# Kernel tuning notes

Hardware: AMD Instinct MI355X
Metric: run time of the kernel (lower is better)

The kernel has to match this reference:

```python
import jax, jax.numpy as jnp
import numpy as np

N_EMBD = 1024
N_HEAD = 16
HEAD_DIM = N_EMBD // N_HEAD
B, T = 2, 2048


def setup_inputs() -> dict:
    key = jax.random.key(0)
    ks = jax.random.split(key, 12)
    s = 0.02
    inp = {
        "x": jax.random.normal(ks[0], (B, T, N_EMBD), dtype=jnp.float32),
        "ln1_g": jnp.ones((N_EMBD,), jnp.float32),
        "ln1_b": jnp.zeros((N_EMBD,), jnp.float32),
        "ln2_g": jnp.ones((N_EMBD,), jnp.float32),
        "ln2_b": jnp.zeros((N_EMBD,), jnp.float32),
        "W_qkv": jax.random.normal(ks[1], (N_EMBD, 3 * N_EMBD), jnp.float32) * s,
        "b_qkv": jnp.zeros((3 * N_EMBD,), jnp.float32),
        "W_o": jax.random.normal(ks[2], (N_EMBD, N_EMBD), jnp.float32) * s,
        "b_o": jnp.zeros((N_EMBD,), jnp.float32),
        "W_fc": jax.random.normal(ks[3], (N_EMBD, 4 * N_EMBD), jnp.float32) * s,
        "b_fc": jnp.zeros((4 * N_EMBD,), jnp.float32),
        "W_proj": jax.random.normal(ks[4], (4 * N_EMBD, N_EMBD), jnp.float32) * s,
        "b_proj": jnp.zeros((N_EMBD,), jnp.float32),
    }
    return inp


def _layernorm(x, g, b, eps=1e-5):
    mu = jnp.mean(x, axis=-1, keepdims=True)
    var = jnp.var(x, axis=-1, keepdims=True)
    return (x - mu) * jax.lax.rsqrt(var + eps) * g + b


def _block(x, ln1_g, ln1_b, ln2_g, ln2_b, W_qkv, b_qkv, W_o, b_o, W_fc, b_fc, W_proj, b_proj):
    # --- attention sub-block (pre-LN) ---
    h = _layernorm(x, ln1_g, ln1_b)
    qkv = h @ W_qkv + b_qkv                     # [B,T,3E]
    q, k, v = jnp.split(qkv, 3, axis=-1)
    def split_heads(t):
        return t.reshape(B, T, N_HEAD, HEAD_DIM).transpose(0, 2, 1, 3)  # [B,H,T,D]
    q, k, v = split_heads(q), split_heads(k), split_heads(v)
    scores = jnp.einsum("bhqd,bhkd->bhqk", q, k) / (HEAD_DIM ** 0.5)
    causal = jnp.tril(jnp.ones((T, T), dtype=bool))
    scores = jnp.where(causal, scores, jnp.float32(-jnp.inf))
    probs = jax.nn.softmax(scores, axis=-1)
    attn = jnp.einsum("bhqk,bhkd->bhqd", probs, v)        # [B,H,T,D]
    attn = attn.transpose(0, 2, 1, 3).reshape(B, T, N_EMBD)
    x = x + attn @ W_o + b_o
    # --- MLP sub-block (pre-LN) ---
    h = _layernorm(x, ln2_g, ln2_b)
    h = jax.nn.gelu(h @ W_fc + b_fc, approximate=False)
    x = x + h @ W_proj + b_proj
    return x


def reference(x, ln1_g, ln1_b, ln2_g, ln2_b, W_qkv, b_qkv, W_o, b_o, W_fc, b_fc, W_proj, b_proj):
    return _block(x, ln1_g, ln1_b, ln2_g, ln2_b, W_qkv, b_qkv, W_o, b_o, W_fc, b_fc, W_proj, b_proj)
```

## Files before the change

kernel.cpp:

```cpp
#include <hip/hip_runtime.h>
#include <hip/hip_bf16.h>


#define TT 2048
#define EE 1024
#define NH 16
#define HD 64

#define AS1 __attribute__((address_space(1)))
#define AS3 __attribute__((address_space(3)))

using bf16x8 = __bf16 __attribute__((ext_vector_type(8)));
using bf16x4 = __bf16 __attribute__((ext_vector_type(4)));
using f32x4  = float __attribute__((ext_vector_type(4)));

template<int N> __device__ __forceinline__ void vm_wait() {
    if constexpr (N == 0)      asm volatile("s_waitcnt vmcnt(0)" ::: "memory");
    else if constexpr (N == 2) asm volatile("s_waitcnt vmcnt(2)" ::: "memory");
    else if constexpr (N == 3) asm volatile("s_waitcnt vmcnt(3)" ::: "memory");
    else if constexpr (N == 4) asm volatile("s_waitcnt vmcnt(4)" ::: "memory");
    else if constexpr (N == 6) asm volatile("s_waitcnt vmcnt(6)" ::: "memory");
    else                       asm volatile("s_waitcnt vmcnt(8)" ::: "memory");
}

__device__ __forceinline__ void barrier_after_dswrite() {
    asm volatile("s_waitcnt lgkmcnt(0)" ::: "memory");
    __builtin_amdgcn_s_barrier();
}
__device__ __forceinline__ void barrier_raw() {
    asm volatile("" ::: "memory");
    __builtin_amdgcn_s_barrier();
}

__device__ __forceinline__ float gelu_fast(float v) {
    float z  = v * 0.70710678118f;
    float az = fabsf(z);
    float t  = __builtin_amdgcn_rcpf(__builtin_fmaf(0.3275911f, az, 1.0f));
    float p  = t * __builtin_fmaf(t,
                   __builtin_fmaf(t,
                     __builtin_fmaf(t,
                       __builtin_fmaf(t, 1.061405429f, -1.453152027f),
                       1.421413741f),
                     -0.284496736f),
                   0.254829592f);
    float e  = __expf(-az * az);
    float er = copysignf(1.0f - p * e, z);
    return 0.5f * v * (1.0f + er);
}

__global__ __launch_bounds__(256) void convt_kernel(const float* __restrict__ W,
                                                    __bf16* __restrict__ WT,
                                                    int K, int N) {
    __shared__ __bf16 t[32][33];
    int n0 = blockIdx.x * 32, k0 = blockIdx.y * 32;
    int tid = threadIdx.x;
    int r = tid >> 3, c4 = (tid & 7) * 4;
    float4 v = *(const float4*)(W + (size_t)(k0 + r) * N + n0 + c4);
    t[r][c4 + 0] = (__bf16)v.x; t[r][c4 + 1] = (__bf16)v.y;
    t[r][c4 + 2] = (__bf16)v.z; t[r][c4 + 3] = (__bf16)v.w;
    __syncthreads();
    bf16x4 o;
    o[0] = t[c4 + 0][r]; o[1] = t[c4 + 1][r];
    o[2] = t[c4 + 2][r]; o[3] = t[c4 + 3][r];
    *(bf16x4*)(WT + (size_t)(n0 + r) * K + k0 + c4) = o;
}

__global__ __launch_bounds__(256) void ln_kernel(const float* __restrict__ x,
                                                 const float* __restrict__ g,
                                                 const float* __restrict__ bta,
                                                 __bf16* __restrict__ out) {
    int row = blockIdx.x;
    int tid = threadIdx.x;
    const float4 xv = *(const float4*)(x + (size_t)row * EE + tid * 4);
    float s  = xv.x + xv.y + xv.z + xv.w;
    float ss = xv.x*xv.x + xv.y*xv.y + xv.z*xv.z + xv.w*xv.w;
    __shared__ float rs[256], rss[256];
    rs[tid] = s; rss[tid] = ss;
    __syncthreads();
    for (int st = 128; st > 0; st >>= 1) {
        if (tid < st) { rs[tid] += rs[tid+st]; rss[tid] += rss[tid+st]; }
        __syncthreads();
    }
    float mean = rs[0] * (1.0f / EE);
    float var  = rss[0] * (1.0f / EE) - mean * mean;
    float rstd = rsqrtf(var + 1e-5f);
    const float4 gv = *(const float4*)(g + tid * 4);
    const float4 bv = *(const float4*)(bta + tid * 4);
    bf16x4 ov;
    ov[0] = (__bf16)((xv.x - mean) * rstd * gv.x + bv.x);
    ov[1] = (__bf16)((xv.y - mean) * rstd * gv.y + bv.y);
    ov[2] = (__bf16)((xv.z - mean) * rstd * gv.z + bv.z);
    ov[3] = (__bf16)((xv.w - mean) * rstd * gv.w + bv.w);
    *(bf16x4*)(out + (size_t)row * EE + tid * 4) = ov;
}

template<int TM, int TN, bool GELU, bool RESID, bool QKV, bool ATOMIC, typename CT>
__global__ __launch_bounds__(256) void gemm_bt_kernel(const __bf16* __restrict__ A,
                                                      const __bf16* __restrict__ BT,
                                                      const float* __restrict__ bias,
                                                      const float* resid, CT* C,
                                                      __bf16* vT,
                                                      int M, int N, int K) {
    constexpr int MT = TM / 32;
    constexpr int NT = TN / 32;
    constexpr int LOADS = TM / 64 + TN / 64;
    constexpr int NBUF  = ATOMIC ? 3 : ((LOADS <= 3) ? 4 : 3);
    constexpr int DEPTH = NBUF - 1;
    constexpr int WAITN = (DEPTH - 1) * LOADS;
    __shared__ __align__(16) __bf16 As[NBUF][TM][32];
    __shared__ __align__(16) __bf16 Bs[NBUF][TN][32];
    int tid = threadIdx.x, wave = tid >> 6, lane = tid & 63;
    int quad = lane >> 4, l16 = lane & 15;
    int wm = wave >> 1, wn = wave & 1;
    int m0 = blockIdx.y * TM, n0 = blockIdx.x * TN;

    const int klen = ATOMIC ? (K >> 1) : K;
    const int koff = ATOMIC ? (int)blockIdx.z * klen : 0;

    f32x4 acc[MT][NT] = {};

    int srow = wave * 16 + (lane >> 2);
    int scol = (((lane & 3) ^ ((lane >> 3) & 3)) * 8);
    int xcol = ((quad ^ ((l16 >> 1) & 3)) * 8);

    auto STAGE = [&](int buf, int kt) {
        int kb = koff + (kt << 5);
#pragma unroll
        for (int p = 0; p < TM / 64; p++) {
            const __bf16* g = A + (size_t)(m0 + p * 64 + srow) * K + kb + scol;
            __builtin_amdgcn_global_load_lds((AS1 const void*)g,
                                             (AS3 void*)&As[buf][p * 64 + wave * 16][0],
                                             16, 0, 0);
        }
#pragma unroll
        for (int p = 0; p < TN / 64; p++) {
            const __bf16* g = BT + (size_t)(n0 + p * 64 + srow) * K + kb + scol;
            __builtin_amdgcn_global_load_lds((AS1 const void*)g,
                                             (AS3 void*)&Bs[buf][p * 64 + wave * 16][0],
                                             16, 0, 0);
        }
    };

    auto COMPUTE = [&](int cur) {
        bf16x8 af[MT], bfr[NT];
#pragma unroll
        for (int mt = 0; mt < MT; mt++)
            af[mt] = *(const bf16x8*)(&As[cur][wm * (MT * 16) + mt * 16 + l16][xcol]);
#pragma unroll
        for (int nt = 0; nt < NT; nt++)
            bfr[nt] = *(const bf16x8*)(&Bs[cur][wn * (NT * 16) + nt * 16 + l16][xcol]);
#pragma unroll
        for (int mt = 0; mt < MT; mt++)
#pragma unroll
            for (int nt = 0; nt < NT; nt++)
                acc[mt][nt] = __builtin_amdgcn_mfma_f32_16x16x32_bf16(af[mt], bfr[nt],
                                                                      acc[mt][nt], 0, 0, 0);
    };

    const int nk = klen >> 5;
#pragma unroll
    for (int i = 0; i < DEPTH; ++i) STAGE(i, i);
    vm_wait<WAITN>();
    __builtin_amdgcn_s_barrier();

    int t = 0;
    for (; t + DEPTH < nk; ++t) {
        STAGE((t + DEPTH) % NBUF, t + DEPTH);
        COMPUTE(t % NBUF);
        vm_wait<WAITN>();
        __builtin_amdgcn_s_barrier();
    }
    for (; t < nk; ++t) {
        COMPUTE(t % NBUF);
        if (t + 1 < nk) {
            int rem = nk - 2 - t;
            if (rem >= 1) vm_wait<LOADS>();
            else          vm_wait<0>();
            __builtin_amdgcn_s_barrier();
        }
    }

#pragma unroll
    for (int nt = 0; nt < NT; nt++) {
        int c = n0 + wn * (NT * 16) + nt * 16 + l16;
        float bv = (!ATOMIC || blockIdx.z == 0) ? bias[c] : 0.0f;
#pragma unroll
        for (int mt = 0; mt < MT; mt++) {
#pragma unroll
            for (int r = 0; r < 4; r++) {
                int row = m0 + wm * (MT * 16) + mt * 16 + quad * 4 + r;
                float v = acc[mt][nt][r] + bv;
                if (GELU)  v = gelu_fast(v);
                if (RESID) v += resid[(size_t)row * N + c];
                if (ATOMIC) {
                    atomicAdd((float*)&C[(size_t)row * N + c], v);
                } else if (!QKV) {
                    C[(size_t)row * N + c] = (CT)v;
                } else {
                    if (c < 2 * EE) {
                        ((__bf16*)C)[(size_t)row * (2 * EE) + c] = (__bf16)v;
                    } else {
                        int cv = c - 2 * EE;
                        int bb = row >> 11, tt = row & (TT - 1);
                        vT[((size_t)(bb * NH + (cv >> 6)) * HD + (cv & 63)) * TT + tt] =
                            (__bf16)v;
                    }
                }
            }
        }
    }
}

__global__ __launch_bounds__(256) void flash_attn_kernel(const __bf16* __restrict__ qkv,
                                                         const __bf16* __restrict__ vT,
                                                         __bf16* __restrict__ out) {
    int h = blockIdx.y, b = blockIdx.z;
    int tid = threadIdx.x, wave = tid >> 6, lane = tid & 63;
    int quad = lane >> 4, l16 = lane & 15;

    __shared__ __align__(16) __bf16 Ks[128 * 72];
    __shared__ __align__(16) __bf16 Ps[4][16 * 136];

    size_t base = (size_t)b * TT * (2 * EE);

    int srow = tid >> 3;
    int scol = (tid & 7) * 8;
    const __bf16* kbase  = qkv + base + EE + h * HD + scol;
    const __bf16* vrow = vT + (size_t)(b * NH + h) * HD * TT + (size_t)l16 * TT + quad * 8;
    __bf16* Psw = &Ps[wave][0];

    int nTiles = (int)gridDim.x * 2;

    for (int pass = 0; pass < 2; pass++) {
        int qt = pass == 0 ? (nTiles - 1 - blockIdx.x) : blockIdx.x;
        int q0 = qt * 64;

        int qrow = q0 + wave * 16 + l16;
        const __bf16* qp = qkv + base + (size_t)qrow * (2 * EE) + h * HD;
        bf16x8 aq0 = *(const bf16x8*)(qp + quad * 8);
        bf16x8 aq1 = *(const bf16x8*)(qp + 32 + quad * 8);

        f32x4 oacc[4] = {};
        float lsum[4] = {0.f, 0.f, 0.f, 0.f};
        int qg_base = q0 + wave * 16 + quad * 4;

        int nIter = (qt >> 1) + 1;

        bf16x8 kr[4];
#pragma unroll
        for (int p = 0; p < 4; p++)
            kr[p] = *(const bf16x8*)(kbase + (size_t)(32 * p + srow) * (2 * EE));
        bf16x8 vf[4][4];
#pragma unroll
        for (int dt = 0; dt < 4; dt++)
#pragma unroll
            for (int w = 0; w < 4; w++)
                vf[dt][w] = *(const bf16x8*)(vrow + (size_t)dt * (16 * TT) + w * 32);

        for (int kt = 0; kt < nIter; ++kt) {
            int k0 = kt * 128;
#pragma unroll
            for (int p = 0; p < 4; p++)
                *(bf16x8*)(&Ks[(32 * p + srow) * 72 + scol]) = kr[p];
            barrier_after_dswrite();

            if (kt < nIter - 1) {
                int kn = k0 + 128;
#pragma unroll
                for (int p = 0; p < 4; p++)
                    kr[p] = *(const bf16x8*)(kbase + (size_t)(kn + 32 * p + srow) * (2 * EE));
            }

            f32x4 s[8];
#pragma unroll
            for (int nt = 0; nt < 8; nt++) {
                bf16x8 bk0 = *(const bf16x8*)(&Ks[(nt * 16 + l16) * 72 + quad * 8]);
                bf16x8 bk1 = *(const bf16x8*)(&Ks[(nt * 16 + l16) * 72 + 32 + quad * 8]);
                f32x4 z = {};
                z = __builtin_amdgcn_mfma_f32_16x16x32_bf16(aq0, bk0, z, 0, 0, 0);
                s[nt] = __builtin_amdgcn_mfma_f32_16x16x32_bf16(aq1, bk1, z, 0, 0, 0);
            }

            bool maskt = (kt == nIter - 1);
#pragma unroll
            for (int nt = 0; nt < 8; nt++) {
                int key = k0 + nt * 16 + l16;
                int cb = 2 * nt + (l16 >> 3);
#pragma unroll
                for (int r = 0; r < 4; r++) {
                    float p;
                    if (maskt && key > qg_base + r) p = 0.0f;
                    else p = __expf(fminf(s[nt][r] * 0.125f, 30.0f));
                    lsum[r] += p;
                    int q = quad * 4 + r;
                    int col = (((cb & 8) | ((cb - 2 * q) & 7)) << 3) | (l16 & 7);
                    Psw[q * 136 + col] = (__bf16)p;
                }
            }

#pragma unroll
            for (int w = 0; w < 4; w++) {
                int cbr = 4 * w + quad;
                int colr = ((cbr & 8) | ((cbr - 2 * l16) & 7)) << 3;
                bf16x8 ap = *(const bf16x8*)(&Psw[l16 * 136 + colr]);
#pragma unroll
                for (int dt = 0; dt < 4; dt++)
                    oacc[dt] = __builtin_amdgcn_mfma_f32_16x16x32_bf16(ap, vf[dt][w],
                                                                       oacc[dt], 0, 0, 0);
            }

            if (kt < nIter - 1) {
                int kn = k0 + 128;
#pragma unroll
                for (int dt = 0; dt < 4; dt++)
#pragma unroll
                    for (int w = 0; w < 4; w++)
                        vf[dt][w] = *(const bf16x8*)(vrow + (size_t)dt * (16 * TT) + kn + w * 32);
            }
            barrier_raw();
        }

#pragma unroll
        for (int off = 1; off < 16; off <<= 1)
#pragma unroll
            for (int r = 0; r < 4; r++) lsum[r] += __shfl_xor(lsum[r], off);
#pragma unroll
        for (int dt = 0; dt < 4; dt++) {
#pragma unroll
            for (int r = 0; r < 4; r++) {
                int qg = qg_base + r;
                out[((size_t)b * TT + qg) * EE + h * HD + dt * 16 + l16] =
                    (__bf16)(oacc[dt][r] / lsum[r]);
            }
        }
    }
}

extern "C" void kernel_launch(void* const* d_in, const int* in_sizes, int n_in,
                              void* d_out, int out_size, void* d_ws, size_t ws_size,
                              hipStream_t stream) {
    const float* x     = (const float*)d_in[0];
    const float* ln1g  = (const float*)d_in[1];
    const float* ln1b  = (const float*)d_in[2];
    const float* ln2g  = (const float*)d_in[3];
    const float* ln2b  = (const float*)d_in[4];
    const float* Wqkv  = (const float*)d_in[5];
    const float* bqkv  = (const float*)d_in[6];
    const float* Wo    = (const float*)d_in[7];
    const float* bo    = (const float*)d_in[8];
    const float* Wfc   = (const float*)d_in[9];
    const float* bfc   = (const float*)d_in[10];
    const float* Wproj = (const float*)d_in[11];
    const float* bproj = (const float*)d_in[12];
    float* out = (float*)d_out;

    const int M = 2 * TT;

    __bf16* ws = (__bf16*)d_ws;
    __bf16* regQ   = ws;
    __bf16* regS   = ws + 16777216;
    __bf16* WfcT   = ws + 20971520;
    __bf16* qkv    = regQ;
    __bf16* vT     = regQ + 8388608;
    __bf16* WqkvT  = regQ + 12582912;
    __bf16* WoT    = regQ + 15728640;
    __bf16* ff     = regQ;
    __bf16* h1 = regS, *atn = regS, *h2 = regS;
    __bf16* WprojT = regS;
    float*  x1 = out;

    convt_kernel<<<dim3(3 * EE / 32, EE / 32), 256, 0, stream>>>(Wqkv, WqkvT, EE, 3 * EE);
    convt_kernel<<<dim3(EE / 32, EE / 32), 256, 0, stream>>>(Wo, WoT, EE, EE);
    convt_kernel<<<dim3(4 * EE / 32, EE / 32), 256, 0, stream>>>(Wfc, WfcT, EE, 4 * EE);

    ln_kernel<<<M, 256, 0, stream>>>(x, ln1g, ln1b, h1);
    gemm_bt_kernel<128, 128, false, false, true, false, __bf16>
        <<<dim3(3 * EE / 128, M / 128), 256, 0, stream>>>(
        h1, WqkvT, bqkv, nullptr, qkv, vT, M, 3 * EE, EE);
    flash_attn_kernel<<<dim3(TT / 128, NH, 2), 256, 0, stream>>>(qkv, vT, atn);
    gemm_bt_kernel<128, 64, false, true, false, false, float>
        <<<dim3(EE / 64, M / 128), 256, 0, stream>>>(
        atn, WoT, bo, x, x1, nullptr, M, EE, EE);
    ln_kernel<<<M, 256, 0, stream>>>(x1, ln2g, ln2b, h2);
    gemm_bt_kernel<128, 128, true, false, false, false, __bf16>
        <<<dim3(4 * EE / 128, M / 128), 256, 0, stream>>>(
        h2, WfcT, bfc, nullptr, ff, nullptr, M, 4 * EE, EE);
    convt_kernel<<<dim3(EE / 32, 4 * EE / 32), 256, 0, stream>>>(Wproj, WprojT, 4 * EE, EE);
    gemm_bt_kernel<128, 64, false, false, false, true, float>
        <<<dim3(EE / 64, M / 128, 2), 256, 0, stream>>>(
        ff, WprojT, bproj, nullptr, out, nullptr, M, EE, 4 * EE);
}
```

Baseline: 453.8 us.

## Split flash attention into single-wave blocks with direct K loads

Measured after the change: 507.1 us. 1.12x slower.

```diff
diff --git a/kernel.cpp b/kernel.cpp
--- a/kernel.cpp
+++ b/kernel.cpp
@@ -21,15 +21,6 @@
     else if constexpr (N == 4) asm volatile("s_waitcnt vmcnt(4)" ::: "memory");
     else if constexpr (N == 6) asm volatile("s_waitcnt vmcnt(6)" ::: "memory");
     else                       asm volatile("s_waitcnt vmcnt(8)" ::: "memory");
-}
-
-__device__ __forceinline__ void barrier_after_dswrite() {
-    asm volatile("s_waitcnt lgkmcnt(0)" ::: "memory");
-    __builtin_amdgcn_s_barrier();
-}
-__device__ __forceinline__ void barrier_raw() {
-    asm volatile("" ::: "memory");
-    __builtin_amdgcn_s_barrier();
 }
 
 __device__ __forceinline__ float gelu_fast(float v) {
@@ -211,127 +202,97 @@
     }
 }
 
-__global__ __launch_bounds__(256) void flash_attn_kernel(const __bf16* __restrict__ qkv,
-                                                         const __bf16* __restrict__ vT,
-                                                         __bf16* __restrict__ out) {
+__global__ __launch_bounds__(64) void flash_attn_kernel(const __bf16* __restrict__ qkv,
+                                                        const __bf16* __restrict__ vT,
+                                                        __bf16* __restrict__ out) {
     int h = blockIdx.y, b = blockIdx.z;
-    int tid = threadIdx.x, wave = tid >> 6, lane = tid & 63;
+    int lane = threadIdx.x & 63;
     int quad = lane >> 4, l16 = lane & 15;
 
-    __shared__ __align__(16) __bf16 Ks[128 * 72];
-    __shared__ __align__(16) __bf16 Ps[4][16 * 136];
+    __shared__ __align__(16) __bf16 Ps[16 * 136];
 
     size_t base = (size_t)b * TT * (2 * EE);
-
-    int srow = tid >> 3;
-    int scol = (tid & 7) * 8;
-    const __bf16* kbase  = qkv + base + EE + h * HD + scol;
+    int qt = (int)gridDim.x - 1 - (int)blockIdx.x;
+    int q0 = qt * 16;
+
+    const __bf16* kb2  = qkv + base + EE + h * HD;
     const __bf16* vrow = vT + (size_t)(b * NH + h) * HD * TT + (size_t)l16 * TT + quad * 8;
-    __bf16* Psw = &Ps[wave][0];
-
-    int nTiles = (int)gridDim.x * 2;
-
-    for (int pass = 0; pass < 2; pass++) {
-        int qt = pass == 0 ? (nTiles - 1 - blockIdx.x) : blockIdx.x;
-        int q0 = qt * 64;
-
-        int qrow = q0 + wave * 16 + l16;
-        const __bf16* qp = qkv + base + (size_t)qrow * (2 * EE) + h * HD;
-        bf16x8 aq0 = *(const bf16x8*)(qp + quad * 8);
-        bf16x8 aq1 = *(const bf16x8*)(qp + 32 + quad * 8);
-
-        f32x4 oacc[4] = {};
-        float lsum[4] = {0.f, 0.f, 0.f, 0.f};
-        int qg_base = q0 + wave * 16 + quad * 4;
-
-        int nIter = (qt >> 1) + 1;
-
-        bf16x8 kr[4];
-#pragma unroll
-        for (int p = 0; p < 4; p++)
-            kr[p] = *(const bf16x8*)(kbase + (size_t)(32 * p + srow) * (2 * EE));
+
+    const __bf16* qp = qkv + base + (size_t)(q0 + l16) * (2 * EE) + h * HD;
+    bf16x8 aq0 = *(const bf16x8*)(qp + quad * 8);
+    bf16x8 aq1 = *(const bf16x8*)(qp + 32 + quad * 8);
+
+    f32x4 oacc[4] = {};
+    float lsum[4] = {0.f, 0.f, 0.f, 0.f};
+    int qg_base = q0 + quad * 4;
+    int nIter = (qt >> 3) + 1;
+
+    for (int kt = 0; kt < nIter; ++kt) {
+        int k0 = kt * 128;
+
+        bf16x8 bk0[8], bk1[8];
+#pragma unroll
+        for (int nt = 0; nt < 8; nt++) {
+            const __bf16* kp = kb2 + (size_t)(k0 + nt * 16 + l16) * (2 * EE) + quad * 8;
+            bk0[nt] = *(const bf16x8*)(kp);
+            bk1[nt] = *(const bf16x8*)(kp + 32);
+        }
+
+        f32x4 s[8];
+#pragma unroll
+        for (int nt = 0; nt < 8; nt++) {
+            f32x4 z = {};
+            z = __builtin_amdgcn_mfma_f32_16x16x32_bf16(aq0, bk0[nt], z, 0, 0, 0);
+            s[nt] = __builtin_amdgcn_mfma_f32_16x16x32_bf16(aq1, bk1[nt], z, 0, 0, 0);
+        }
+
         bf16x8 vf[4][4];
 #pragma unroll
         for (int dt = 0; dt < 4; dt++)
 #pragma unroll
             for (int w = 0; w < 4; w++)
-                vf[dt][w] = *(const bf16x8*)(vrow + (size_t)dt * (16 * TT) + w * 32);
-
-        for (int kt = 0; kt < nIter; ++kt) {
-            int k0 = kt * 128;
-#pragma unroll
-            for (int p = 0; p < 4; p++)
-                *(bf16x8*)(&Ks[(32 * p + srow) * 72 + scol]) = kr[p];
-            barrier_after_dswrite();
-
-            if (kt < nIter - 1) {
-                int kn = k0 + 128;
-#pragma unroll
-                for (int p = 0; p < 4; p++)
-                    kr[p] = *(const bf16x8*)(kbase + (size_t)(kn + 32 * p + srow) * (2 * EE));
+                vf[dt][w] = *(const bf16x8*)(vrow + (size_t)dt * (16 * TT) + k0 + w * 32);
+
+        bool maskt = (kt == nIter - 1);
+#pragma unroll
+        for (int nt = 0; nt < 8; nt++) {
+            int key = k0 + nt * 16 + l16;
+            int cb = 2 * nt + (l16 >> 3);
+#pragma unroll
+            for (int r = 0; r < 4; r++) {
+                float p;
+                if (maskt && key > qg_base + r) p = 0.0f;
+                else p = __expf(fminf(s[nt][r] * 0.125f, 30.0f));
+                lsum[r] += p;
+                int q = quad * 4 + r;
+                int col = (((cb & 8) | ((cb - 2 * q) & 7)) << 3) | (l16 & 7);
+                Ps[q * 136 + col] = (__bf16)p;
             }
-
-            f32x4 s[8];
-#pragma unroll
-            for (int nt = 0; nt < 8; nt++) {
-                bf16x8 bk0 = *(const bf16x8*)(&Ks[(nt * 16 + l16) * 72 + quad * 8]);
-                bf16x8 bk1 = *(const bf16x8*)(&Ks[(nt * 16 + l16) * 72 + 32 + quad * 8]);
-                f32x4 z = {};
-                z = __builtin_amdgcn_mfma_f32_16x16x32_bf16(aq0, bk0, z, 0, 0, 0);
-                s[nt] = __builtin_amdgcn_mfma_f32_16x16x32_bf16(aq1, bk1, z, 0, 0, 0);
-            }
-
-            bool maskt = (kt == nIter - 1);
-#pragma unroll
-            for (int nt = 0; nt < 8; nt++) {
-                int key = k0 + nt * 16 + l16;
-                int cb = 2 * nt + (l16 >> 3);
-#pragma unroll
-                for (int r = 0; r < 4; r++) {
-                    float p;
-                    if (maskt && key > qg_base + r) p = 0.0f;
-                    else p = __expf(fminf(s[nt][r] * 0.125f, 30.0f));
-                    lsum[r] += p;
-                    int q = quad * 4 + r;
-                    int col = (((cb & 8) | ((cb - 2 * q) & 7)) << 3) | (l16 & 7);
-                    Psw[q * 136 + col] = (__bf16)p;
-                }
-            }
-
-#pragma unroll
-            for (int w = 0; w < 4; w++) {
-                int cbr = 4 * w + quad;
-                int colr = ((cbr & 8) | ((cbr - 2 * l16) & 7)) << 3;
-                bf16x8 ap = *(const bf16x8*)(&Psw[l16 * 136 + colr]);
-#pragma unroll
-                for (int dt = 0; dt < 4; dt++)
-                    oacc[dt] = __builtin_amdgcn_mfma_f32_16x16x32_bf16(ap, vf[dt][w],
-                                                                       oacc[dt], 0, 0, 0);
-            }
-
-            if (kt < nIter - 1) {
-                int kn = k0 + 128;
-#pragma unroll
-                for (int dt = 0; dt < 4; dt++)
-#pragma unroll
-                    for (int w = 0; w < 4; w++)
-                        vf[dt][w] = *(const bf16x8*)(vrow + (size_t)dt * (16 * TT) + kn + w * 32);
-            }
-            barrier_raw();
-        }
-
-#pragma unroll
-        for (int off = 1; off < 16; off <<= 1)
-#pragma unroll
-            for (int r = 0; r < 4; r++) lsum[r] += __shfl_xor(lsum[r], off);
-#pragma unroll
-        for (int dt = 0; dt < 4; dt++) {
-#pragma unroll
-            for (int r = 0; r < 4; r++) {
-                int qg = qg_base + r;
-                out[((size_t)b * TT + qg) * EE + h * HD + dt * 16 + l16] =
-                    (__bf16)(oacc[dt][r] / lsum[r]);
-            }
+        }
+
+#pragma unroll
+        for (int w = 0; w < 4; w++) {
+            int cbr = 4 * w + quad;
+            int colr = ((cbr & 8) | ((cbr - 2 * l16) & 7)) << 3;
+            bf16x8 ap = *(const bf16x8*)(&Ps[l16 * 136 + colr]);
+#pragma unroll
+            for (int dt = 0; dt < 4; dt++)
+                oacc[dt] = __builtin_amdgcn_mfma_f32_16x16x32_bf16(ap, vf[dt][w],
+                                                                   oacc[dt], 0, 0, 0);
+        }
+    }
+
+#pragma unroll
+    for (int off = 1; off < 16; off <<= 1)
+#pragma unroll
+        for (int r = 0; r < 4; r++) lsum[r] += __shfl_xor(lsum[r], off);
+#pragma unroll
+    for (int dt = 0; dt < 4; dt++) {
+#pragma unroll
+        for (int r = 0; r < 4; r++) {
+            int qg = qg_base + r;
+            out[((size_t)b * TT + qg) * EE + h * HD + dt * 16 + l16] =
+                (__bf16)(oacc[dt][r] / lsum[r]);
         }
     }
 }
@@ -377,7 +338,7 @@
     gemm_bt_kernel<128, 128, false, false, true, false, __bf16>
         <<<dim3(3 * EE / 128, M / 128), 256, 0, stream>>>(
         h1, WqkvT, bqkv, nullptr, qkv, vT, M, 3 * EE, EE);
-    flash_attn_kernel<<<dim3(TT / 128, NH, 2), 256, 0, stream>>>(qkv, vT, atn);
+    flash_attn_kernel<<<dim3(TT / 16, NH, 2), 64, 0, stream>>>(qkv, vT, atn);
     gemm_bt_kernel<128, 64, false, true, false, false, float>
         <<<dim3(EE / 64, M / 128), 256, 0, stream>>>(
         atn, WoT, bo, x, x1, nullptr, M, EE, EE);
```
